# Kernel optimization log

Hardware: AMD Instinct MI355X
Metric: run time of the kernel (lower is better)

## Reference

```python
import jax, jax.numpy as jnp
import numpy as np

N, E, IN_DIM, H, D = 100000, 1600000, 128, 4, 32


def setup_inputs() -> dict:
    key = jax.random.key(0)
    ks = jax.random.split(key, 8)
    glorot = lambda k, shape: jax.random.uniform(
        k, shape, jnp.float32, -1.0, 1.0) * np.sqrt(6.0 / (shape[0] + shape[1]))
    return {
        "x": jax.random.normal(ks[0], (N, IN_DIM), jnp.float32),
        "row": jax.random.randint(ks[1], (E,), 0, N, jnp.int32),
        "col": jax.random.randint(ks[2], (E,), 0, N, jnp.int32),
        "W_l": glorot(ks[3], (IN_DIM, H * D)),
        "W_r": glorot(ks[4], (IN_DIM, H * D)),
        "a1w": glorot(ks[5], (IN_DIM, H)),
        "a2w": glorot(ks[6], (IN_DIM, H)),
        "bias": jnp.zeros((H * D,), jnp.float32),
    }


def reference(x, row, col, W_l, W_r, a1w, a2w, bias):
    n = x.shape[0]  # num_nodes (= graph[0].max()+1 with dense random rows)
    x_l = (x @ W_l).reshape(n, H, D)          # [N,H,D]
    x_r = x @ W_r                              # [N,H*D]
    # per-edge attention logits: a1[row] + a2[col], leaky-relu(0.2)
    attn = jax.nn.leaky_relu((x @ a1w)[row] + (x @ a2w)[col], 0.2)  # [E,H]
    # segment softmax over destination rows (numerically stable)
    m = jax.ops.segment_max(attn, row, num_segments=n)               # [N,H]
    e = jnp.exp(attn - m[row])
    s = jax.ops.segment_sum(e, row, num_segments=n)                  # [N,H]
    attn_d = e / s[row]                                              # [E,H]
    # per-head SpMM: scatter-add weighted source features to destinations
    msgs = attn_d[:, :, None] * x_l[col]                             # [E,H,D]
    out = jax.ops.segment_sum(msgs, row, num_segments=n).reshape(n, H * D)
    return out + x_r + bias
```

## Files before the change

kernel.cpp:

```cpp
#include <hip/hip_runtime.h>


typedef short bfvec8 __attribute__((ext_vector_type(8)));
typedef float f32x4  __attribute__((ext_vector_type(4)));

#define BK 256
#define CAP 6144
#define EPB 4096
#define REC 272

__device__ __forceinline__ unsigned short f2bf(float f) {
  union { float f; unsigned int i; } v; v.f = f;
  unsigned int r = v.i + 0x7fffu + ((v.i >> 16) & 1u);
  return (unsigned short)(r >> 16);
}

__global__ __launch_bounds__(128) void wprep_k(
    const float* __restrict__ Wl, const float* __restrict__ Wr,
    const float* __restrict__ a1w, const float* __restrict__ a2w,
    unsigned short* __restrict__ Wtg)
{
  const int n = blockIdx.x;
  const int y = blockIdx.y;
  const int k = threadIdx.x;
  const float* W = y ? Wr : Wl;
  const float* A = y ? a2w : a1w;
  const float LOG2E = 1.4426950408889634f;
  float v = (n < 128) ? W[(size_t)k * 128 + n] : A[k * 4 + (n - 128)] * LOG2E;
  Wtg[((size_t)y * 132 + n) * 128 + k] = f2bf(v);
}

__global__ __launch_bounds__(256) void gemm_mfma(
    const float* __restrict__ x, const unsigned short* __restrict__ Wtg,
    const float* __restrict__ bias,
    char* __restrict__ xls, float* __restrict__ out,
    float* __restrict__ s1, int N)
{
  __shared__ unsigned short xs[64][136];
  __shared__ unsigned short Ws[132][136];
  const int t = threadIdx.x;
  const int n0 = blockIdx.x * 64;
  const int y = blockIdx.y;
  const unsigned short* Wt = Wtg + (size_t)y * 132 * 128;

  for (int i = t; i < 2048; i += 256) {
    int rr = i >> 5, kc = (i & 31) << 2;
    float4 v = make_float4(0.f, 0.f, 0.f, 0.f);
    int n = n0 + rr;
    if (n < N) v = *(const float4*)&x[(size_t)n * 128 + kc];
    unsigned int lo = (unsigned int)f2bf(v.x) | ((unsigned int)f2bf(v.y) << 16);
    unsigned int hi = (unsigned int)f2bf(v.z) | ((unsigned int)f2bf(v.w) << 16);
    *(uint2*)&xs[rr][kc] = make_uint2(lo, hi);
  }
  for (int i = t; i < 2112; i += 256) {
    int nr = i >> 4, kc = (i & 15) << 3;
    *(uint4*)&Ws[nr][kc] = *(const uint4*)&Wt[(size_t)nr * 128 + kc];
  }
  __syncthreads();

  const int w    = t >> 6;
  const int lane = t & 63;
  const int m    = lane & 15;
  const int quad = lane >> 4;

  f32x4 acc[9];
  #pragma unroll
  for (int i = 0; i < 9; ++i) acc[i] = (f32x4){0.f, 0.f, 0.f, 0.f};

  #pragma unroll
  for (int kc = 0; kc < 128; kc += 32) {
    bfvec8 af = *(const bfvec8*)&xs[16 * w + m][kc + quad * 8];
    #pragma unroll
    for (int nt = 0; nt < 9; ++nt) {
      int nr = nt * 16 + m; if (nr > 131) nr = 131;
      bfvec8 bfr = *(const bfvec8*)&Ws[nr][kc + quad * 8];
      acc[nt] = __builtin_amdgcn_mfma_f32_16x16x32_bf16(af, bfr, acc[nt], 0, 0, 0);
    }
  }

  #pragma unroll
  for (int nt = 0; nt < 8; ++nt) {
    int c = nt * 16 + m;
    float b = y ? bias[c] : 0.f;
    #pragma unroll
    for (int r = 0; r < 4; ++r) {
      int n = n0 + 16 * w + quad * 4 + r;
      if (n < N) {
        float v = acc[nt][r] + b;
        if (y) out[(size_t)n * 128 + c] = v;
        else   *(unsigned short*)(xls + (size_t)n * REC + 2 * c) = f2bf(v);
      }
    }
  }
  if (m < 4) {
    #pragma unroll
    for (int r = 0; r < 4; ++r) {
      int n = n0 + 16 * w + quad * 4 + r;
      if (n < N) {
        if (y) *(float*)(xls + (size_t)n * REC + 256 + 4 * m) = acc[8][r];
        else   s1[n * 4 + m] = acc[8][r];
      }
    }
  }
}

__global__ __launch_bounds__(512) void init_k(int* __restrict__ bcur, int NBK) {
  int b = threadIdx.x;
  if (b < NBK) bcur[b] = b * CAP;
}

__global__ __launch_bounds__(256) void bin_k(const int* __restrict__ row,
    const int* __restrict__ col, int* __restrict__ bcur,
    unsigned int* __restrict__ binned, int E, int NBK)
{
  __shared__ int h[512];
  __shared__ int base[512];
  const int t = threadIdx.x;
  const int e0 = blockIdx.x * EPB;
  const int e1 = min(e0 + EPB, E);

  for (int i = t; i < NBK; i += 256) h[i] = 0;
  __syncthreads();
  for (int e = e0 + t; e < e1; e += 256)
    atomicAdd(&h[row[e] >> 8], 1);
  __syncthreads();
  for (int i = t; i < NBK; i += 256) {
    int c = h[i];
    base[i] = c ? atomicAdd(&bcur[i], c) : 0;
  }
  __syncthreads();
  for (int i = t; i < NBK; i += 256) h[i] = 0;
  __syncthreads();
  for (int e = e0 + t; e < e1; e += 256) {
    int r = row[e];
    unsigned c = (unsigned)col[e];
    int b = r >> 8;
    int rk = atomicAdd(&h[b], 1);
    binned[base[b] + rk] = ((unsigned)(r & 255) << 17) | c;
  }
}

__global__ __launch_bounds__(256) void csr_k(const unsigned int* __restrict__ binned,
    const int* __restrict__ bcur, int* __restrict__ offs, int* __restrict__ deg,
    unsigned int* __restrict__ colsort, int N)
{
  __shared__ int h[BK];
  __shared__ int sh[BK];
  const int t = threadIdx.x;
  const int b = blockIdx.x;
  const int lo = b * BK;
  const int e0 = b * CAP;
  const int e1 = bcur[b];

  h[t] = 0;
  __syncthreads();
  for (int i = e0 + t; i < e1; i += 256)
    atomicAdd(&h[binned[i] >> 17], 1);
  __syncthreads();

  int v = h[t];
  sh[t] = v;
  __syncthreads();
  for (int off = 1; off < 256; off <<= 1) {
    int tv = (t >= off) ? sh[t - off] : 0;
    __syncthreads();
    sh[t] += tv;
    __syncthreads();
  }
  int ex = sh[t] - v;
  int node = lo + t;
  if (node < N) { offs[node] = e0 + ex; deg[node] = v; }

  h[t] = ex;
  __syncthreads();
  for (int i = e0 + t; i < e1; i += 256) {
    unsigned p = binned[i];
    int rlo = p >> 17;
    unsigned c = p & 0x1FFFFu;
    int pos = atomicAdd(&h[rlo], 1);
    colsort[e0 + pos] = c * REC;
  }
}

__global__ __launch_bounds__(256) void agg_k(const int* __restrict__ offs,
    const int* __restrict__ deg, const unsigned int* __restrict__ colsort,
    const float* __restrict__ s1, const char* __restrict__ xls,
    float* __restrict__ out, int N)
{
  const int lane = threadIdx.x & 63;
  const int n = blockIdx.x * 4 + (threadIdx.x >> 6);
  if (n >= N) return;
  const int e0 = offs[n], e1 = e0 + deg[n];
  const int h = lane >> 4;
  const float s1h = s1[n * 4 + h];
  const unsigned lane4 = (unsigned)(lane << 2);
  const unsigned h256 = 256u + (unsigned)(h << 2);

  float acc0 = 0.f, acc1 = 0.f, wsum = 0.f;
  int i0 = e0;
  for (; i0 + 8 <= e1; i0 += 8) {
    unsigned cs[8];
    #pragma unroll
    for (int j = 0; j < 8; ++j) cs[j] = colsort[i0 + j];
    float z2v[8]; unsigned pv[8];
    #pragma unroll
    for (int j = 0; j < 8; ++j) {
      z2v[j] = *(const float*)(xls + (cs[j] + h256));
      pv[j]  = *(const unsigned*)(xls + (cs[j] + lane4));
    }
    #pragma unroll
    for (int j = 0; j < 8; ++j) {
      float z = s1h + z2v[j];
      z = fmaxf(z, 0.2f * z);
      float wv = exp2f(z);
      wsum += wv;
      union { unsigned u; float f; } lo, hi;
      lo.u = pv[j] << 16;
      hi.u = pv[j] & 0xffff0000u;
      acc0 += wv * lo.f;
      acc1 += wv * hi.f;
    }
  }
  for (; i0 < e1; ++i0) {
    unsigned cs = colsort[i0];
    float z2 = *(const float*)(xls + (cs + h256));
    unsigned p = *(const unsigned*)(xls + (cs + lane4));
    float z = s1h + z2;
    z = fmaxf(z, 0.2f * z);
    float wv = exp2f(z);
    wsum += wv;
    union { unsigned u; float f; } lo, hi;
    lo.u = p << 16; hi.u = p & 0xffff0000u;
    acc0 += wv * lo.f;
    acc1 += wv * hi.f;
  }

  float inv = (wsum > 0.f) ? (1.0f / wsum) : 0.f;
  const size_t o = (size_t)n * 128 + 2 * lane;
  float2 xr = *(const float2*)&out[o];
  float2 res; res.x = acc0 * inv + xr.x; res.y = acc1 * inv + xr.y;
  *(float2*)&out[o] = res;
}

extern "C" void kernel_launch(void* const* d_in, const int* in_sizes, int n_in,
                              void* d_out, int out_size, void* d_ws, size_t ws_size,
                              hipStream_t stream) {
  const float* x    = (const float*)d_in[0];
  const int*   row  = (const int*)d_in[1];
  const int*   col  = (const int*)d_in[2];
  const float* Wl   = (const float*)d_in[3];
  const float* Wr   = (const float*)d_in[4];
  const float* a1w  = (const float*)d_in[5];
  const float* a2w  = (const float*)d_in[6];
  const float* bias = (const float*)d_in[7];
  float* out = (float*)d_out;
  const int N = in_sizes[0] / 128;
  const int E = in_sizes[1];
  (void)n_in; (void)out_size; (void)ws_size;

  const int NBK = (N + BK - 1) / BK;

  char* ws = (char*)d_ws;
  size_t off = 0;
  auto carve = [&](size_t bytes) { void* p = ws + off; off += (bytes + 255) & ~(size_t)255; return p; };
  char* xls            = (char*)carve((size_t)N * REC);
  float* s1            = (float*)carve((size_t)N * 4 * 4);
  int* offs            = (int*)carve((size_t)N * 4);
  int* deg             = (int*)carve((size_t)N * 4);
  unsigned int* colsort= (unsigned int*)carve((size_t)NBK * CAP * 4);
  unsigned int* binned = (unsigned int*)carve((size_t)NBK * CAP * 4);
  int* bcur            = (int*)carve((size_t)NBK * 4);
  unsigned short* Wtg  = (unsigned short*)carve((size_t)2 * 132 * 128 * 2);

  wprep_k  <<<dim3(132, 2), 128, 0, stream>>>(Wl, Wr, a1w, a2w, Wtg);
  gemm_mfma<<<dim3((N + 63) / 64, 2), 256, 0, stream>>>(x, Wtg, bias, xls, out, s1, N);
  init_k   <<<1, 512, 0, stream>>>(bcur, NBK);
  bin_k    <<<(E + EPB - 1) / EPB, 256, 0, stream>>>(row, col, bcur, binned, E, NBK);
  csr_k    <<<NBK, 256, 0, stream>>>(binned, bcur, offs, deg, colsort, N);
  agg_k    <<<(N + 3) / 4, 256, 0, stream>>>(offs, deg, colsort, s1, xls, out, N);
}
```

Baseline: 316.1 us.

## Fuse both GEMM halves per block, cache rows in bin_k, share attention weights via shuffles

```diff
diff --git a/kernel.cpp b/kernel.cpp
--- a/kernel.cpp
+++ b/kernel.cpp
@@ -40,8 +40,6 @@
   __shared__ unsigned short Ws[132][136];
   const int t = threadIdx.x;
   const int n0 = blockIdx.x * 64;
-  const int y = blockIdx.y;
-  const unsigned short* Wt = Wtg + (size_t)y * 132 * 128;
 
   for (int i = t; i < 2048; i += 256) {
     int rr = i >> 5, kc = (i & 31) << 2;
@@ -52,53 +50,59 @@
     unsigned int hi = (unsigned int)f2bf(v.z) | ((unsigned int)f2bf(v.w) << 16);
     *(uint2*)&xs[rr][kc] = make_uint2(lo, hi);
   }
-  for (int i = t; i < 2112; i += 256) {
-    int nr = i >> 4, kc = (i & 15) << 3;
-    *(uint4*)&Ws[nr][kc] = *(const uint4*)&Wt[(size_t)nr * 128 + kc];
-  }
-  __syncthreads();
 
   const int w    = t >> 6;
   const int lane = t & 63;
   const int m    = lane & 15;
   const int quad = lane >> 4;
 
-  f32x4 acc[9];
   #pragma unroll
-  for (int i = 0; i < 9; ++i) acc[i] = (f32x4){0.f, 0.f, 0.f, 0.f};
-
-  #pragma unroll
-  for (int kc = 0; kc < 128; kc += 32) {
-    bfvec8 af = *(const bfvec8*)&xs[16 * w + m][kc + quad * 8];
-    #pragma unroll
-    for (int nt = 0; nt < 9; ++nt) {
-      int nr = nt * 16 + m; if (nr > 131) nr = 131;
-      bfvec8 bfr = *(const bfvec8*)&Ws[nr][kc + quad * 8];
-      acc[nt] = __builtin_amdgcn_mfma_f32_16x16x32_bf16(af, bfr, acc[nt], 0, 0, 0);
-    }
-  }
-
-  #pragma unroll
-  for (int nt = 0; nt < 8; ++nt) {
-    int c = nt * 16 + m;
-    float b = y ? bias[c] : 0.f;
-    #pragma unroll
-    for (int r = 0; r < 4; ++r) {
-      int n = n0 + 16 * w + quad * 4 + r;
-      if (n < N) {
-        float v = acc[nt][r] + b;
-        if (y) out[(size_t)n * 128 + c] = v;
-        else   *(unsigned short*)(xls + (size_t)n * REC + 2 * c) = f2bf(v);
+  for (int y = 0; y < 2; ++y) {
+    const unsigned short* Wt = Wtg + (size_t)y * 132 * 128;
+    if (y) __syncthreads();
+    for (int i = t; i < 2112; i += 256) {
+      int nr = i >> 4, kc = (i & 15) << 3;
+      *(uint4*)&Ws[nr][kc] = *(const uint4*)&Wt[(size_t)nr * 128 + kc];
+    }
+    __syncthreads();
+
+    f32x4 acc[9];
+    #pragma unroll
+    for (int i = 0; i < 9; ++i) acc[i] = (f32x4){0.f, 0.f, 0.f, 0.f};
+
+    #pragma unroll
+    for (int kc = 0; kc < 128; kc += 32) {
+      bfvec8 af = *(const bfvec8*)&xs[16 * w + m][kc + quad * 8];
+      #pragma unroll
+      for (int nt = 0; nt < 9; ++nt) {
+        int nr = nt * 16 + m; if (nr > 131) nr = 131;
+        bfvec8 bfr = *(const bfvec8*)&Ws[nr][kc + quad * 8];
+        acc[nt] = __builtin_amdgcn_mfma_f32_16x16x32_bf16(af, bfr, acc[nt], 0, 0, 0);
       }
     }
-  }
-  if (m < 4) {
-    #pragma unroll
-    for (int r = 0; r < 4; ++r) {
-      int n = n0 + 16 * w + quad * 4 + r;
-      if (n < N) {
-        if (y) *(float*)(xls + (size_t)n * REC + 256 + 4 * m) = acc[8][r];
-        else   s1[n * 4 + m] = acc[8][r];
+
+    #pragma unroll
+    for (int nt = 0; nt < 8; ++nt) {
+      int c = nt * 16 + m;
+      float b = y ? bias[c] : 0.f;
+      #pragma unroll
+      for (int r = 0; r < 4; ++r) {
+        int n = n0 + 16 * w + quad * 4 + r;
+        if (n < N) {
+          float v = acc[nt][r] + b;
+          if (y) out[(size_t)n * 128 + c] = v;
+          else   *(unsigned short*)(xls + (size_t)n * REC + 2 * c) = f2bf(v);
+        }
+      }
+    }
+    if (m < 4) {
+      #pragma unroll
+      for (int r = 0; r < 4; ++r) {
+        int n = n0 + 16 * w + quad * 4 + r;
+        if (n < N) {
+          if (y) *(float*)(xls + (size_t)n * REC + 256 + 4 * m) = acc[8][r];
+          else   s1[n * 4 + m] = acc[8][r];
+        }
       }
     }
   }
@@ -119,10 +123,15 @@
   const int e0 = blockIdx.x * EPB;
   const int e1 = min(e0 + EPB, E);
 
+  int rloc[16];
   for (int i = t; i < NBK; i += 256) h[i] = 0;
   __syncthreads();
-  for (int e = e0 + t; e < e1; e += 256)
-    atomicAdd(&h[row[e] >> 8], 1);
+  #pragma unroll
+  for (int k = 0; k < 16; ++k) {
+    int e = e0 + t + (k << 8);
+    rloc[k] = (e < e1) ? row[e] : -1;
+    if (rloc[k] >= 0) atomicAdd(&h[rloc[k] >> 8], 1);
+  }
   __syncthreads();
   for (int i = t; i < NBK; i += 256) {
     int c = h[i];
@@ -131,12 +140,16 @@
   __syncthreads();
   for (int i = t; i < NBK; i += 256) h[i] = 0;
   __syncthreads();
-  for (int e = e0 + t; e < e1; e += 256) {
-    int r = row[e];
-    unsigned c = (unsigned)col[e];
-    int b = r >> 8;
-    int rk = atomicAdd(&h[b], 1);
-    binned[base[b] + rk] = ((unsigned)(r & 255) << 17) | c;
+  #pragma unroll
+  for (int k = 0; k < 16; ++k) {
+    int e = e0 + t + (k << 8);
+    if (e < e1) {
+      int r = rloc[k];
+      unsigned c = (unsigned)col[e];
+      int b = r >> 8;
+      int rk = atomicAdd(&h[b], 1);
+      binned[base[b] + rk] = ((unsigned)(r & 255) << 17) | c;
+    }
   }
 }
 
@@ -191,34 +204,41 @@
   const int n = blockIdx.x * 4 + (threadIdx.x >> 6);
   if (n >= N) return;
   const int e0 = offs[n], e1 = e0 + deg[n];
-  const int h = lane >> 4;
+  const int h  = lane >> 4;
+  const int hp = lane & 3;
+  const int jj = (lane >> 2) & 7;
   const float s1h = s1[n * 4 + h];
+  const float s1c = s1[n * 4 + hp];
   const unsigned lane4 = (unsigned)(lane << 2);
-  const unsigned h256 = 256u + (unsigned)(h << 2);
+  const unsigned h256  = 256u + (unsigned)(h << 2);
+  const unsigned hp256 = 256u + (unsigned)(hp << 2);
 
   float acc0 = 0.f, acc1 = 0.f, wsum = 0.f;
   int i0 = e0;
   for (; i0 + 8 <= e1; i0 += 8) {
+    unsigned csl = colsort[i0 + jj];
+    float z2 = *(const float*)(xls + (csl + hp256));
+    float z = s1c + z2;
+    z = fmaxf(z, 0.2f * z);
+    float wv = exp2f(z);
+
     unsigned cs[8];
     #pragma unroll
     for (int j = 0; j < 8; ++j) cs[j] = colsort[i0 + j];
-    float z2v[8]; unsigned pv[8];
+    unsigned pv[8];
+    #pragma unroll
+    for (int j = 0; j < 8; ++j)
+      pv[j] = *(const unsigned*)(xls + (cs[j] + lane4));
+
     #pragma unroll
     for (int j = 0; j < 8; ++j) {
-      z2v[j] = *(const float*)(xls + (cs[j] + h256));
-      pv[j]  = *(const unsigned*)(xls + (cs[j] + lane4));
-    }
-    #pragma unroll
-    for (int j = 0; j < 8; ++j) {
-      float z = s1h + z2v[j];
-      z = fmaxf(z, 0.2f * z);
-      float wv = exp2f(z);
-      wsum += wv;
+      float wj = __shfl(wv, (j << 2) | h);
+      wsum += wj;
       union { unsigned u; float f; } lo, hi;
       lo.u = pv[j] << 16;
       hi.u = pv[j] & 0xffff0000u;
-      acc0 += wv * lo.f;
-      acc1 += wv * hi.f;
+      acc0 += wj * lo.f;
+      acc1 += wj * hi.f;
     }
   }
   for (; i0 < e1; ++i0) {
@@ -273,7 +293,7 @@
   unsigned short* Wtg  = (unsigned short*)carve((size_t)2 * 132 * 128 * 2);
 
   wprep_k  <<<dim3(132, 2), 128, 0, stream>>>(Wl, Wr, a1w, a2w, Wtg);
-  gemm_mfma<<<dim3((N + 63) / 64, 2), 256, 0, stream>>>(x, Wtg, bias, xls, out, s1, N);
+  gemm_mfma<<<(N + 63) / 64, 256, 0, stream>>>(x, Wtg, bias, xls, out, s1, N);
   init_k   <<<1, 512, 0, stream>>>(bcur, NBK);
   bin_k    <<<(E + EPB - 1) / EPB, 256, 0, stream>>>(row, col, bcur, binned, E, NBK);
   csr_k    <<<NBK, 256, 0, stream>>>(binned, bcur, offs, deg, colsort, N);
```

Measured after the change: 302.5 us. 1.04x faster.
